# Kernel tuning notes

Hardware: AMD Instinct MI355X
Metric: run time of the kernel (lower is better)

Reference implementation:

```python
import jax, jax.numpy as jnp
import numpy as np

B, S, HID, NH, HD = 2, 8192, 768, 12, 64
BLOCK, NRAND = 64, 3


def _make_attn_indices():
    # Mirrors SparseSelfAttention.bigbird_attention index construction:
    # globals = first block + last block tokens; randoms = NRAND per block.
    rng = np.random.default_rng(0)
    glob = np.concatenate([np.arange(BLOCK), np.arange(S - BLOCK, S)])
    rand = [rng.permutation(BLOCK)[:NRAND] + i * BLOCK for i in range(S // BLOCK)]
    idx = np.unique(np.concatenate([glob] + rand))
    return jnp.asarray(idx, dtype=jnp.int32)


def setup_inputs() -> dict:
    key = jax.random.key(0)
    ks = jax.random.split(key, 6)
    w = lambda k: jax.random.normal(k, (HID, HID), jnp.float32) * 0.02
    return {
        "hidden_states": jax.random.normal(ks[0], (B, S, HID), jnp.float32),
        "attn_indices": _make_attn_indices(),
        "Wq": w(ks[1]), "bq": jnp.zeros((HID,), jnp.float32),
        "Wk": w(ks[2]), "bk": jnp.zeros((HID,), jnp.float32),
        "Wv": w(ks[3]), "bv": jnp.zeros((HID,), jnp.float32),
        "Wo": w(ks[4]), "bo": jnp.zeros((HID,), jnp.float32),
    }


def reference(hidden_states, attn_indices, Wq, bq, Wk, bk, Wv, bv, Wo, bo):
    # torch nn.Linear: y = x @ W.T + b
    heads = lambda x: x.reshape(B, S, NH, HD).transpose(0, 2, 1, 3)  # [B,H,S,d]
    q = heads(hidden_states @ Wq.T + bq)
    k = heads(hidden_states @ Wk.T + bk)
    v = heads(hidden_states @ Wv.T + bv)

    sel_q = q[:, :, attn_indices]  # gather selected queries [B,H,Nsel,d]
    scores = jnp.einsum('bhqd,bhkd->bhqk', sel_q, k) / jnp.sqrt(jnp.float32(HD))
    probs = jax.nn.softmax(scores, axis=-1)              # [B,H,Nsel,S]
    ctx = jnp.einsum('bhqk,bhkd->bhqd', probs, v)        # [B,H,Nsel,d]

    # scatter back into zeros (non-selected query positions stay zero)
    full = jnp.zeros_like(q).at[:, :, attn_indices].set(ctx)
    context = full.transpose(0, 2, 1, 3).reshape(B, S, HID)
    output = context @ Wo.T + bo
    return (output, probs)
```

## Files before the change

### kernel.cpp

```cpp
#include <hip/hip_runtime.h>
#include <hip/hip_bf16.h>

#define B_   2
#define S_   8192
#define HID_ 768
#define NH_  12
#define HD_  64

#define KC1 512
#define NC1 (S_ / KC1)
#define KC2 1024
#define NC2 (S_ / KC2)

typedef __attribute__((ext_vector_type(8))) short short8;
typedef __attribute__((ext_vector_type(4))) float f32x4;

__device__ __forceinline__ ushort f2b(float x) {
    __hip_bfloat16 h = __float2bfloat16(x);
    return *reinterpret_cast<ushort*>(&h);
}

__device__ __forceinline__ int swzb(int row, int colbyte, int rowbytes) {
    return row * rowbytes + (colbyte ^ ((row & 7) << 4));
}

__device__ __forceinline__ void glds16(const ushort* g, ushort* l) {
    __builtin_amdgcn_global_load_lds(
        (__attribute__((address_space(1))) unsigned int*)g,
        (__attribute__((address_space(3))) unsigned int*)l, 16, 0, 0);
}

__global__ void fill_bias_kernel(float* __restrict__ out, const float* __restrict__ bo) {
    const int total = B_ * S_ * (HID_ / 4);
    const float4* b4 = reinterpret_cast<const float4*>(bo);
    float4* o4 = reinterpret_cast<float4*>(out);
    for (int i = blockIdx.x * blockDim.x + threadIdx.x; i < total; i += gridDim.x * blockDim.x) {
        o4[i] = b4[i % (HID_ / 4)];
    }
}

__global__ void f32_to_bf16_kernel(const float* __restrict__ in, ushort* __restrict__ out,
                                   int n4, float scale) {
    const float4* i4 = reinterpret_cast<const float4*>(in);
    ushort4* o4 = reinterpret_cast<ushort4*>(out);
    for (int i = blockIdx.x * blockDim.x + threadIdx.x; i < n4; i += gridDim.x * blockDim.x) {
        float4 v = i4[i];
        ushort4 o;
        o.x = f2b(v.x * scale);
        o.y = f2b(v.y * scale);
        o.z = f2b(v.z * scale);
        o.w = f2b(v.w * scale);
        o4[i] = o;
    }
}

__global__ void gather_qb_kernel(const ushort* __restrict__ Hb, const int* __restrict__ idx,
                                 ushort* __restrict__ Qinb, int nq, int nqpad) {
    int m = blockIdx.x;
    int b = m / nqpad, qi = m - b * nqpad;
    uint4* dst = reinterpret_cast<uint4*>(Qinb + (size_t)m * HID_);
    if (qi < nq) {
        int srow = b * S_ + idx[qi];
        const uint4* src = reinterpret_cast<const uint4*>(Hb + (size_t)srow * HID_);
        dst[threadIdx.x] = src[threadIdx.x];
    } else {
        dst[threadIdx.x] = make_uint4(0, 0, 0, 0);
    }
}

enum { GST_KV = 0, GST_PLAIN = 1 };

template<int MODE>
__launch_bounds__(256)
__global__ void gemm_bf16_kernel(const ushort* __restrict__ A, const ushort* __restrict__ W,
                                 const float* __restrict__ bias, float bscale,
                                 ushort* __restrict__ C) {
    __shared__ __align__(16) ushort As[128 * 64];
    __shared__ __align__(16) ushort Ws[128 * 64];
    const int t = threadIdx.x;
    const int lane = t & 63, w = t >> 6;
    const int wr = w >> 1, wc = w & 1;
    const int m0 = blockIdx.x * 128;
    const int n0 = blockIdx.y * 128;

    f32x4 acc[4][4];
    #pragma unroll
    for (int i = 0; i < 4; ++i)
        #pragma unroll
        for (int j = 0; j < 4; ++j) acc[i][j] = (f32x4){0.f, 0.f, 0.f, 0.f};

    for (int k0 = 0; k0 < HID_; k0 += 64) {
        __syncthreads();
        #pragma unroll
        for (int it = 0; it < 4; ++it) {
            int sid = t + it * 256;
            int row = sid >> 3, seg = sid & 7;
            int cb = (seg * 16) ^ ((row & 7) << 4);
            glds16(A + (size_t)(m0 + row) * HID_ + k0 + cb / 2, (ushort*)((char*)As + sid * 16));
            glds16(W + (size_t)(n0 + row) * HID_ + k0 + cb / 2, (ushort*)((char*)Ws + sid * 16));
        }
        __syncthreads();

        short8 af[4][2], bf_[4][2];
        #pragma unroll
        for (int mi = 0; mi < 4; ++mi)
            #pragma unroll
            for (int kh = 0; kh < 2; ++kh)
                af[mi][kh] = *reinterpret_cast<const short8*>(
                    (char*)As + swzb(wr * 64 + mi * 16 + (lane & 15), (lane >> 4) * 16 + kh * 64, 128));
        #pragma unroll
        for (int ni = 0; ni < 4; ++ni)
            #pragma unroll
            for (int kh = 0; kh < 2; ++kh)
                bf_[ni][kh] = *reinterpret_cast<const short8*>(
                    (char*)Ws + swzb(wc * 64 + ni * 16 + (lane & 15), (lane >> 4) * 16 + kh * 64, 128));

        #pragma unroll
        for (int mi = 0; mi < 4; ++mi)
            #pragma unroll
            for (int ni = 0; ni < 4; ++ni) {
                acc[mi][ni] = __builtin_amdgcn_mfma_f32_16x16x32_bf16(af[mi][0], bf_[ni][0], acc[mi][ni], 0, 0, 0);
                acc[mi][ni] = __builtin_amdgcn_mfma_f32_16x16x32_bf16(af[mi][1], bf_[ni][1], acc[mi][ni], 0, 0, 0);
            }
    }

    float bl[4];
    #pragma unroll
    for (int ni = 0; ni < 4; ++ni)
        bl[ni] = bias[n0 + wc * 64 + ni * 16 + (lane & 15)] * bscale;

    #pragma unroll
    for (int mi = 0; mi < 4; ++mi) {
        #pragma unroll
        for (int ni = 0; ni < 4; ++ni) {
            int n = n0 + wc * 64 + ni * 16 + (lane & 15);
            #pragma unroll
            for (int r = 0; r < 4; ++r) {
                int m = m0 + wr * 64 + mi * 16 + (lane >> 4) * 4 + r;
                ushort val = f2b(acc[mi][ni][r] + bl[ni]);
                if (MODE == GST_KV) {
                    int b = m >> 13, s = m & (S_ - 1);
                    int h = n >> 6, d = n & 63;
                    C[(((size_t)(b * NH_ + h)) * S_ + s) * HD_ + d] = val;
                } else {
                    C[(size_t)m * HID_ + n] = val;
                }
            }
        }
    }
}

__launch_bounds__(256)
__global__ void gemm64_scatter(const float* __restrict__ A, const float* __restrict__ W,
                               const float* __restrict__ bias, float* __restrict__ Cf,
                               int M, const int* __restrict__ idx, int nq) {
    __shared__ float As[16][68];
    __shared__ float Ws[16][68];
    const int t  = threadIdx.x;
    const int m0 = blockIdx.x * 64;
    const int n0 = blockIdx.y * 64;
    const int tm = t >> 4, tn = t & 15;

    float acc[4][4];
    #pragma unroll
    for (int i = 0; i < 4; ++i)
        #pragma unroll
        for (int j = 0; j < 4; ++j) acc[i][j] = 0.f;

    const int fr = t >> 2, fc = t & 3;
    for (int k0 = 0; k0 < HID_; k0 += 16) {
        float4 av = make_float4(0.f, 0.f, 0.f, 0.f);
        if (m0 + fr < M) av = *reinterpret_cast<const float4*>(&A[(size_t)(m0 + fr) * HID_ + k0 + fc * 4]);
        float4 wv = *reinterpret_cast<const float4*>(&W[(size_t)(n0 + fr) * HID_ + k0 + fc * 4]);
        As[fc * 4 + 0][fr] = av.x;
        As[fc * 4 + 1][fr] = av.y;
        As[fc * 4 + 2][fr] = av.z;
        As[fc * 4 + 3][fr] = av.w;
        Ws[fc * 4 + 0][fr] = wv.x;
        Ws[fc * 4 + 1][fr] = wv.y;
        Ws[fc * 4 + 2][fr] = wv.z;
        Ws[fc * 4 + 3][fr] = wv.w;
        __syncthreads();
        #pragma unroll
        for (int kk = 0; kk < 16; ++kk) {
            float4 a4 = *reinterpret_cast<const float4*>(&As[kk][tm * 4]);
            float4 w4 = *reinterpret_cast<const float4*>(&Ws[kk][tn * 4]);
            float a[4] = {a4.x, a4.y, a4.z, a4.w};
            float ww[4] = {w4.x, w4.y, w4.z, w4.w};
            #pragma unroll
            for (int i = 0; i < 4; ++i)
                #pragma unroll
                for (int j = 0; j < 4; ++j)
                    acc[i][j] = fmaf(a[i], ww[j], acc[i][j]);
        }
        __syncthreads();
    }

    float bl[4];
    #pragma unroll
    for (int j = 0; j < 4; ++j) bl[j] = bias[n0 + tn * 4 + j];

    #pragma unroll
    for (int i = 0; i < 4; ++i) {
        int m = m0 + tm * 4 + i;
        if (m >= M) continue;
        int b = m / nq, qi = m - b * nq;
        int srow = b * S_ + idx[qi];
        float* p = &Cf[(size_t)srow * HID_ + n0 + tn * 4];
        *reinterpret_cast<float4*>(p) =
            make_float4(acc[i][0] + bl[0], acc[i][1] + bl[1], acc[i][2] + bl[2], acc[i][3] + bl[3]);
    }
}

__global__ void transpose_v_kernel(const ushort* __restrict__ V, ushort* __restrict__ Vt) {
    __shared__ ushort tile[64][72];
    int bh = blockIdx.y;
    int k0 = blockIdx.x * 64;
    int t = threadIdx.x;
    const ushort* src = V + (size_t)bh * S_ * HD_ + (size_t)k0 * HD_;
    #pragma unroll
    for (int it = 0; it < 2; ++it) {
        int sid = t + it * 256;
        int key = sid >> 3, seg = sid & 7;
        *reinterpret_cast<uint4*>(&tile[key][seg * 8]) =
            *reinterpret_cast<const uint4*>(src + (size_t)key * HD_ + seg * 8);
    }
    __syncthreads();
    ushort* dst = Vt + (size_t)bh * HD_ * S_ + k0;
    #pragma unroll
    for (int it = 0; it < 2; ++it) {
        int sid = t + it * 256;
        int d = sid >> 3, seg = sid & 7;
        ushort tmp[8];
        #pragma unroll
        for (int j = 0; j < 8; ++j) tmp[j] = tile[seg * 8 + j][d];
        *reinterpret_cast<uint4*>(dst + (size_t)d * S_ + seg * 8) = *reinterpret_cast<uint4*>(tmp);
    }
}

__launch_bounds__(512)
__global__ void attn_pass1_mfma(const ushort* __restrict__ Qsel, const ushort* __restrict__ Kb,
                                float2* __restrict__ mlp, int nq, int nqpad) {
    __shared__ __align__(16) ushort Ks[128 * 64];
    const int t = threadIdx.x;
    const int lane = t & 63, w = t >> 6;
    const int bh = blockIdx.z;
    const int b = bh / NH_, h = bh - b * NH_;
    const int q0 = blockIdx.x * 128;
    const int chunk = blockIdx.y;

    const ushort* qp = Qsel + (size_t)(b * nqpad + q0 + 16 * w + (lane & 15)) * HID_
                       + h * HD_ + (lane >> 4) * 8;
    short8 qa0 = *reinterpret_cast<const short8*>(qp);
    short8 qa1 = *reinterpret_cast<const short8*>(qp + 32);

    float m_r[4], l_r[4];
    #pragma unroll
    for (int r = 0; r < 4; ++r) { m_r[r] = -1e30f; l_r[r] = 0.f; }

    const ushort* kbase = Kb + (size_t)bh * S_ * HD_;

    for (int kb = 0; kb < KC1; kb += 128) {
        int k0 = chunk * KC1 + kb;
        __syncthreads();
        #pragma unroll
        for (int it = 0; it < 2; ++it) {
            int sid = t + it * 512;
            int row = sid >> 3, seg = sid & 7;
            int cb = (seg * 16) ^ ((row & 7) << 4);
            glds16(kbase + (size_t)(k0 + row) * HD_ + cb / 2, (ushort*)((char*)Ks + sid * 16));
        }
        __syncthreads();

        f32x4 sf[8];
        #pragma unroll
        for (int ns = 0; ns < 8; ++ns) {
            short8 b0 = *reinterpret_cast<const short8*>((char*)Ks + swzb(ns * 16 + (lane & 15), (lane >> 4) * 16, 128));
            short8 b1 = *reinterpret_cast<const short8*>((char*)Ks + swzb(ns * 16 + (lane & 15), (lane >> 4) * 16 + 64, 128));
            f32x4 acc = {0.f, 0.f, 0.f, 0.f};
            acc = __builtin_amdgcn_mfma_f32_16x16x32_bf16(qa0, b0, acc, 0, 0, 0);
            acc = __builtin_amdgcn_mfma_f32_16x16x32_bf16(qa1, b1, acc, 0, 0, 0);
            sf[ns] = acc;
        }

        #pragma unroll
        for (int r = 0; r < 4; ++r) {
            float bm = sf[0][r];
            #pragma unroll
            for (int ns = 1; ns < 8; ++ns) bm = fmaxf(bm, sf[ns][r]);
            float mn = fmaxf(m_r[r], bm);
            float sum = 0.f;
            #pragma unroll
            for (int ns = 0; ns < 8; ++ns) sum += __expf(sf[ns][r] - mn);
            l_r[r] = l_r[r] * __expf(m_r[r] - mn) + sum;
            m_r[r] = mn;
        }
    }

    #pragma unroll
    for (int r = 0; r < 4; ++r) {
        float m = m_r[r], l = l_r[r];
        #pragma unroll
        for (int off = 1; off < 16; off <<= 1) {
            float om = __shfl_xor(m, off);
            float ol = __shfl_xor(l, off);
            float mn = fmaxf(m, om);
            l = l * __expf(m - mn) + ol * __expf(om - mn);
            m = mn;
        }
        if ((lane & 15) == 0) {
            int row = q0 + 16 * w + 4 * (lane >> 4) + r;
            mlp[(size_t)chunk * (B_ * NH_ * nqpad) + (size_t)bh * nqpad + row] = make_float2(m, l);
        }
    }
}

__global__ void ml_reduce_kernel(const float2* __restrict__ mlp, float2* __restrict__ ml, int nqpad) {
    int i = blockIdx.x * blockDim.x + threadIdx.x;
    int total = B_ * NH_ * nqpad;
    if (i >= total) return;
    float m = -1e30f, l = 0.f;
    #pragma unroll
    for (int c = 0; c < NC1; ++c) {
        float2 v = mlp[(size_t)c * total + i];
        float mn = fmaxf(m, v.x);
        l = l * __expf(m - mn) + v.y * __expf(v.x - mn);
        m = mn;
    }
    ml[i] = make_float2(m, l);
}

__launch_bounds__(512)
__global__ void attn_pass2_mfma(const ushort* __restrict__ Qsel, const ushort* __restrict__ Kb,
                                const ushort* __restrict__ Vtb, const float2* __restrict__ ml,
                                float* __restrict__ probs, float* __restrict__ ctxp, int nq, int nqpad) {
    __shared__ __align__(16) ushort Ks[128 * 64];
    __shared__ __align__(16) ushort Vs[64 * 128];
    __shared__ __align__(16) ushort Ps[128 * 128];
    __shared__ float mls[128], ils[128];
    const int t = threadIdx.x;
    const int lane = t & 63, w = t >> 6;
    const int bh = blockIdx.z;
    const int b = bh / NH_, h = bh - b * NH_;
    const int q0 = blockIdx.x * 128;
    const int chunk = blockIdx.y;

    const ushort* qp = Qsel + (size_t)(b * nqpad + q0 + 16 * w + (lane & 15)) * HID_
                       + h * HD_ + (lane >> 4) * 8;
    short8 qa0 = *reinterpret_cast<const short8*>(qp);
    short8 qa1 = *reinterpret_cast<const short8*>(qp + 32);

    if (t < 128) {
        float2 v = ml[(size_t)bh * nqpad + q0 + t];
        mls[t] = v.x;
        ils[t] = 1.f / v.y;
    }

    const ushort* kbase  = Kb  + (size_t)bh * S_ * HD_;
    const ushort* vtbase = Vtb + (size_t)bh * HD_ * S_;
    const size_t prow0 = (size_t)bh * nq;

    f32x4 accc[4];
    #pragma unroll
    for (int d = 0; d < 4; ++d) accc[d] = (f32x4){0.f, 0.f, 0.f, 0.f};

    float mr[4], ilr[4];
    bool mload = false;

    for (int kb = 0; kb < KC2; kb += 128) {
        int k0 = chunk * KC2 + kb;
        __syncthreads();
        #pragma unroll
        for (int it = 0; it < 2; ++it) {
            int sid = t + it * 512;
            int row = sid >> 3, seg = sid & 7;
            int cb = (seg * 16) ^ ((row & 7) << 4);
            glds16(kbase + (size_t)(k0 + row) * HD_ + cb / 2, (ushort*)((char*)Ks + sid * 16));
        }
        #pragma unroll
        for (int it = 0; it < 2; ++it) {
            int sid = t + it * 512;
            int row = sid >> 4, seg = sid & 15;
            int cb = (seg * 16) ^ ((row & 7) << 4);
            glds16(vtbase + (size_t)row * S_ + k0 + cb / 2, (ushort*)((char*)Vs + sid * 16));
        }
        __syncthreads();
        if (!mload) {
            #pragma unroll
            for (int r = 0; r < 4; ++r) {
                int rl = 16 * w + 4 * (lane >> 4) + r;
                mr[r] = mls[rl];
                ilr[r] = ils[rl];
            }
            mload = true;
        }

        #pragma unroll
        for (int ns = 0; ns < 8; ++ns) {
            short8 b0 = *reinterpret_cast<const short8*>((char*)Ks + swzb(ns * 16 + (lane & 15), (lane >> 4) * 16, 128));
            short8 b1 = *reinterpret_cast<const short8*>((char*)Ks + swzb(ns * 16 + (lane & 15), (lane >> 4) * 16 + 64, 128));
            f32x4 acc = {0.f, 0.f, 0.f, 0.f};
            acc = __builtin_amdgcn_mfma_f32_16x16x32_bf16(qa0, b0, acc, 0, 0, 0);
            acc = __builtin_amdgcn_mfma_f32_16x16x32_bf16(qa1, b1, acc, 0, 0, 0);
            #pragma unroll
            for (int r = 0; r < 4; ++r) {
                int rl = 16 * w + 4 * (lane >> 4) + r;
                float p = __expf(acc[r] - mr[r]) * ilr[r];
                int qrow = q0 + rl;
                if (qrow < nq)
                    probs[(prow0 + qrow) * (size_t)S_ + k0 + ns * 16 + (lane & 15)] = p;
                *reinterpret_cast<ushort*>((char*)Ps + swzb(rl, (ns * 16 + (lane & 15)) * 2, 256)) = f2b(p);
            }
        }

        short8 pa[4];
        #pragma unroll
        for (int ks = 0; ks < 4; ++ks)
            pa[ks] = *reinterpret_cast<const short8*>((char*)Ps + swzb(16 * w + (lane & 15), ks * 64 + (lane >> 4) * 16, 256));
        #pragma unroll
        for (int ds = 0; ds < 4; ++ds) {
            #pragma unroll
            for (int ks = 0; ks < 4; ++ks) {
                short8 vb = *reinterpret_cast<const short8*>((char*)Vs + swzb(ds * 16 + (lane & 15), ks * 64 + (lane >> 4) * 16, 256));
                accc[ds] = __builtin_amdgcn_mfma_f32_16x16x32_bf16(pa[ks], vb, accc[ds], 0, 0, 0);
            }
        }
    }

    float* dst = ctxp + (size_t)chunk * ((size_t)B_ * nq * HID_);
    #pragma unroll
    for (int ds = 0; ds < 4; ++ds) {
        #pragma unroll
        for (int r = 0; r < 4; ++r) {
            int qrow = q0 + 16 * w + 4 * (lane >> 4) + r;
            if (qrow < nq)
                dst[(size_t)(b * nq + qrow) * HID_ + h * HD_ + ds * 16 + (lane & 15)] = accc[ds][r];
        }
    }
}

__global__ void ctx_reduce_kernel(const float* __restrict__ ctxp, float* __restrict__ ctx, int Mq) {
    const int n4 = Mq * (HID_ / 4);
    const float4* src = reinterpret_cast<const float4*>(ctxp);
    float4* dst = reinterpret_cast<float4*>(ctx);
    for (int i = blockIdx.x * blockDim.x + threadIdx.x; i < n4; i += gridDim.x * blockDim.x) {
        float4 s = make_float4(0.f, 0.f, 0.f, 0.f);
        #pragma unroll
        for (int c = 0; c < NC2; ++c) {
            float4 v = src[(size_t)c * n4 + i];
            s.x += v.x; s.y += v.y; s.z += v.z; s.w += v.w;
        }
        dst[i] = s;
    }
}

extern "C" void kernel_launch(void* const* d_in, const int* in_sizes, int n_in,
                              void* d_out, int out_size, void* d_ws, size_t ws_size,
                              hipStream_t stream) {
    const float* hidden = (const float*)d_in[0];
    const int*   idx    = (const int*)d_in[1];
    const float* Wq = (const float*)d_in[2];
    const float* bq = (const float*)d_in[3];
    const float* Wk = (const float*)d_in[4];
    const float* bk = (const float*)d_in[5];
    const float* Wv = (const float*)d_in[6];
    const float* bv = (const float*)d_in[7];
    const float* Wo = (const float*)d_in[8];
    const float* bo = (const float*)d_in[9];
    const int nq = in_sizes[1];
    const int qt128 = (nq + 127) / 128;
    const int nqpad = qt128 * 128;
    const int Mq = B_ * nq;
    const int Mqp = B_ * nqpad;

    float* out   = (float*)d_out;
    float* probs = out + (size_t)B_ * S_ * HID_;

    char* ws = (char*)d_ws;
    const size_t kvN = (size_t)B_ * NH_ * S_ * HD_;
    ushort* Hb    = (ushort*)ws;                 ws += kvN * 2;
    ushort* K_buf = (ushort*)ws;                 ws += kvN * 2;
    ushort* V_buf = (ushort*)ws;                 ws += kvN * 2;
    ushort* Vt    = (ushort*)ws;                 ws += kvN * 2;
    ushort* Wkb   = (ushort*)ws;                 ws += (size_t)HID_ * HID_ * 2;
    ushort* Wvb   = (ushort*)ws;                 ws += (size_t)HID_ * HID_ * 2;
    ushort* Wqb   = (ushort*)ws;                 ws += (size_t)HID_ * HID_ * 2;
    ushort* Qinb  = (ushort*)ws;                 ws += (size_t)Mqp * HID_ * 2;
    ushort* Qsel  = (ushort*)ws;                 ws += (size_t)Mqp * HID_ * 2;
    float*  ctxb  = (float*)ws;                  ws += (size_t)Mq * HID_ * 4;
    float*  ctxp  = (float*)ws;                  ws += (size_t)NC2 * Mq * HID_ * 4;
    float2* mlp   = (float2*)ws;                 ws += (size_t)NC1 * B_ * NH_ * nqpad * 8;
    float2* ml    = (float2*)ws;                 ws += (size_t)B_ * NH_ * nqpad * 8;

    fill_bias_kernel<<<2048, 256, 0, stream>>>(out, bo);

    f32_to_bf16_kernel<<<2048, 256, 0, stream>>>(hidden, Hb, (int)(kvN / 4), 1.0f);
    const int wn4 = HID_ * HID_ / 4;
    f32_to_bf16_kernel<<<576, 256, 0, stream>>>(Wk, Wkb, wn4, 1.0f);
    f32_to_bf16_kernel<<<576, 256, 0, stream>>>(Wv, Wvb, wn4, 1.0f);
    f32_to_bf16_kernel<<<576, 256, 0, stream>>>(Wq, Wqb, wn4, 0.125f);

    gather_qb_kernel<<<Mqp, 96, 0, stream>>>(Hb, idx, Qinb, nq, nqpad);

    dim3 gKV(B_ * S_ / 128, HID_ / 128);
    gemm_bf16_kernel<GST_KV><<<gKV, 256, 0, stream>>>(Hb, Wkb, bk, 1.0f, K_buf);
    gemm_bf16_kernel<GST_KV><<<gKV, 256, 0, stream>>>(Hb, Wvb, bv, 1.0f, V_buf);

    transpose_v_kernel<<<dim3(S_ / 64, B_ * NH_), 256, 0, stream>>>(V_buf, Vt);

    dim3 gQ(Mqp / 128, HID_ / 128);
    gemm_bf16_kernel<GST_PLAIN><<<gQ, 256, 0, stream>>>(Qinb, Wqb, bq, 0.125f, Qsel);

    dim3 gA1(nqpad / 128, NC1, B_ * NH_);
    attn_pass1_mfma<<<gA1, 512, 0, stream>>>(Qsel, K_buf, mlp, nq, nqpad);

    int totalml = B_ * NH_ * nqpad;
    ml_reduce_kernel<<<(totalml + 255) / 256, 256, 0, stream>>>(mlp, ml, nqpad);

    dim3 gA2(nqpad / 128, NC2, B_ * NH_);
    attn_pass2_mfma<<<gA2, 512, 0, stream>>>(Qsel, K_buf, Vt, ml, probs, ctxp, nq, nqpad);

    ctx_reduce_kernel<<<1024, 256, 0, stream>>>(ctxp, ctxb, Mq);

    dim3 gO((Mq + 63) / 64, HID_ / 64);
    gemm64_scatter<<<gO, 256, 0, stream>>>(ctxb, Wo, bo, out, Mq, idx, nq);
}
```

Before: 338.4 us.

## Loop all query tiles per block in attention, bf16 MFMA output GEMM, fuse weight casts

Each attention block (pass 1 and pass 2) now loops over up to four 128-row query tiles. This reuses each K/V tile loaded into shared memory across all queries instead of reloading it once per query tile. Pass 2 chunk size drops to 512 to keep enough blocks in flight. The fp32 SIMT output projection is replaced by the bf16 MFMA GEMM with a scatter epilogue, so the context reduce now emits bf16 and Wo is also converted. The four weight conversions are merged into one launch. The risks are higher register pressure and a hard cap of 512 selected queries, since more would silently drop tiles.

```diff
diff --git a/kernel.cpp b/kernel.cpp
--- a/kernel.cpp
+++ b/kernel.cpp
@@ -9,7 +9,7 @@
 
 #define KC1 512
 #define NC1 (S_ / KC1)
-#define KC2 1024
+#define KC2 512
 #define NC2 (S_ / KC2)
 
 typedef __attribute__((ext_vector_type(8))) short short8;
@@ -54,6 +54,28 @@
     }
 }
 
+__global__ void conv_weights_kernel(const float* __restrict__ Wk, const float* __restrict__ Wv,
+                                    const float* __restrict__ Wq, const float* __restrict__ Wo,
+                                    ushort* __restrict__ Wkb, ushort* __restrict__ Wvb,
+                                    ushort* __restrict__ Wqb, ushort* __restrict__ Wob) {
+    int which = blockIdx.y;
+    const float* src = which == 0 ? Wk : (which == 1 ? Wv : (which == 2 ? Wq : Wo));
+    ushort* dst = which == 0 ? Wkb : (which == 1 ? Wvb : (which == 2 ? Wqb : Wob));
+    float scale = (which == 2) ? 0.125f : 1.0f;
+    const int n4 = HID_ * HID_ / 4;
+    const float4* i4 = reinterpret_cast<const float4*>(src);
+    ushort4* o4 = reinterpret_cast<ushort4*>(dst);
+    for (int i = blockIdx.x * blockDim.x + threadIdx.x; i < n4; i += gridDim.x * blockDim.x) {
+        float4 v = i4[i];
+        ushort4 o;
+        o.x = f2b(v.x * scale);
+        o.y = f2b(v.y * scale);
+        o.z = f2b(v.z * scale);
+        o.w = f2b(v.w * scale);
+        o4[i] = o;
+    }
+}
+
 __global__ void gather_qb_kernel(const ushort* __restrict__ Hb, const int* __restrict__ idx,
                                  ushort* __restrict__ Qinb, int nq, int nqpad) {
     int m = blockIdx.x;
@@ -68,13 +90,14 @@
     }
 }
 
-enum { GST_KV = 0, GST_PLAIN = 1 };
+enum { GST_KV = 0, GST_PLAIN = 1, GST_SCATF32 = 2 };
 
 template<int MODE>
 __launch_bounds__(256)
 __global__ void gemm_bf16_kernel(const ushort* __restrict__ A, const ushort* __restrict__ W,
                                  const float* __restrict__ bias, float bscale,
-                                 ushort* __restrict__ C) {
+                                 ushort* __restrict__ C, float* __restrict__ Cf,
+                                 const int* __restrict__ idx, int nq, int Mq) {
     __shared__ __align__(16) ushort As[128 * 64];
     __shared__ __align__(16) ushort Ws[128 * 64];
     const int t = threadIdx.x;
@@ -137,78 +160,22 @@
             #pragma unroll
             for (int r = 0; r < 4; ++r) {
                 int m = m0 + wr * 64 + mi * 16 + (lane >> 4) * 4 + r;
-                ushort val = f2b(acc[mi][ni][r] + bl[ni]);
+                float fv = acc[mi][ni][r] + bl[ni];
                 if (MODE == GST_KV) {
                     int b = m >> 13, s = m & (S_ - 1);
                     int h = n >> 6, d = n & 63;
-                    C[(((size_t)(b * NH_ + h)) * S_ + s) * HD_ + d] = val;
+                    C[(((size_t)(b * NH_ + h)) * S_ + s) * HD_ + d] = f2b(fv);
+                } else if (MODE == GST_PLAIN) {
+                    C[(size_t)m * HID_ + n] = f2b(fv);
                 } else {
-                    C[(size_t)m * HID_ + n] = val;
+                    if (m < Mq) {
+                        int b = m / nq, qi = m - b * nq;
+                        int srow = b * S_ + idx[qi];
+                        Cf[(size_t)srow * HID_ + n] = fv;
+                    }
                 }
             }
         }
-    }
-}
-
-__launch_bounds__(256)
-__global__ void gemm64_scatter(const float* __restrict__ A, const float* __restrict__ W,
-                               const float* __restrict__ bias, float* __restrict__ Cf,
-                               int M, const int* __restrict__ idx, int nq) {
-    __shared__ float As[16][68];
-    __shared__ float Ws[16][68];
-    const int t  = threadIdx.x;
-    const int m0 = blockIdx.x * 64;
-    const int n0 = blockIdx.y * 64;
-    const int tm = t >> 4, tn = t & 15;
-
-    float acc[4][4];
-    #pragma unroll
-    for (int i = 0; i < 4; ++i)
-        #pragma unroll
-        for (int j = 0; j < 4; ++j) acc[i][j] = 0.f;
-
-    const int fr = t >> 2, fc = t & 3;
-    for (int k0 = 0; k0 < HID_; k0 += 16) {
-        float4 av = make_float4(0.f, 0.f, 0.f, 0.f);
-        if (m0 + fr < M) av = *reinterpret_cast<const float4*>(&A[(size_t)(m0 + fr) * HID_ + k0 + fc * 4]);
-        float4 wv = *reinterpret_cast<const float4*>(&W[(size_t)(n0 + fr) * HID_ + k0 + fc * 4]);
-        As[fc * 4 + 0][fr] = av.x;
-        As[fc * 4 + 1][fr] = av.y;
-        As[fc * 4 + 2][fr] = av.z;
-        As[fc * 4 + 3][fr] = av.w;
-        Ws[fc * 4 + 0][fr] = wv.x;
-        Ws[fc * 4 + 1][fr] = wv.y;
-        Ws[fc * 4 + 2][fr] = wv.z;
-        Ws[fc * 4 + 3][fr] = wv.w;
-        __syncthreads();
-        #pragma unroll
-        for (int kk = 0; kk < 16; ++kk) {
-            float4 a4 = *reinterpret_cast<const float4*>(&As[kk][tm * 4]);
-            float4 w4 = *reinterpret_cast<const float4*>(&Ws[kk][tn * 4]);
-            float a[4] = {a4.x, a4.y, a4.z, a4.w};
-            float ww[4] = {w4.x, w4.y, w4.z, w4.w};
-            #pragma unroll
-            for (int i = 0; i < 4; ++i)
-                #pragma unroll
-                for (int j = 0; j < 4; ++j)
-                    acc[i][j] = fmaf(a[i], ww[j], acc[i][j]);
-        }
-        __syncthreads();
-    }
-
-    float bl[4];
-    #pragma unroll
-    for (int j = 0; j < 4; ++j) bl[j] = bias[n0 + tn * 4 + j];
-
-    #pragma unroll
-    for (int i = 0; i < 4; ++i) {
-        int m = m0 + tm * 4 + i;
-        if (m >= M) continue;
-        int b = m / nq, qi = m - b * nq;
-        int srow = b * S_ + idx[qi];
-        float* p = &Cf[(size_t)srow * HID_ + n0 + tn * 4];
-        *reinterpret_cast<float4*>(p) =
-            make_float4(acc[i][0] + bl[0], acc[i][1] + bl[1], acc[i][2] + bl[2], acc[i][3] + bl[3]);
     }
 }
 
@@ -244,19 +211,26 @@
     __shared__ __align__(16) ushort Ks[128 * 64];
     const int t = threadIdx.x;
     const int lane = t & 63, w = t >> 6;
-    const int bh = blockIdx.z;
+    const int chunk = blockIdx.x, bh = blockIdx.y;
     const int b = bh / NH_, h = bh - b * NH_;
-    const int q0 = blockIdx.x * 128;
-    const int chunk = blockIdx.y;
-
-    const ushort* qp = Qsel + (size_t)(b * nqpad + q0 + 16 * w + (lane & 15)) * HID_
-                       + h * HD_ + (lane >> 4) * 8;
-    short8 qa0 = *reinterpret_cast<const short8*>(qp);
-    short8 qa1 = *reinterpret_cast<const short8*>(qp + 32);
-
-    float m_r[4], l_r[4];
-    #pragma unroll
-    for (int r = 0; r < 4; ++r) { m_r[r] = -1e30f; l_r[r] = 0.f; }
+    const int nqt = nqpad >> 7;
+
+    short8 qa[4][2];
+    #pragma unroll
+    for (int qt = 0; qt < 4; ++qt) {
+        if (qt < nqt) {
+            const ushort* qp = Qsel + (size_t)(b * nqpad + qt * 128 + 16 * w + (lane & 15)) * HID_
+                               + h * HD_ + (lane >> 4) * 8;
+            qa[qt][0] = *reinterpret_cast<const short8*>(qp);
+            qa[qt][1] = *reinterpret_cast<const short8*>(qp + 32);
+        }
+    }
+
+    float m_r[4][4], l_r[4][4];
+    #pragma unroll
+    for (int qt = 0; qt < 4; ++qt)
+        #pragma unroll
+        for (int r = 0; r < 4; ++r) { m_r[qt][r] = -1e30f; l_r[qt][r] = 0.f; }
 
     const ushort* kbase = Kb + (size_t)bh * S_ * HD_;
 
@@ -272,45 +246,59 @@
         }
         __syncthreads();
 
-        f32x4 sf[8];
+        short8 kf[8][2];
         #pragma unroll
         for (int ns = 0; ns < 8; ++ns) {
-            short8 b0 = *reinterpret_cast<const short8*>((char*)Ks + swzb(ns * 16 + (lane & 15), (lane >> 4) * 16, 128));
-            short8 b1 = *reinterpret_cast<const short8*>((char*)Ks + swzb(ns * 16 + (lane & 15), (lane >> 4) * 16 + 64, 128));
-            f32x4 acc = {0.f, 0.f, 0.f, 0.f};
-            acc = __builtin_amdgcn_mfma_f32_16x16x32_bf16(qa0, b0, acc, 0, 0, 0);
-            acc = __builtin_amdgcn_mfma_f32_16x16x32_bf16(qa1, b1, acc, 0, 0, 0);
-            sf[ns] = acc;
-        }
-
+            kf[ns][0] = *reinterpret_cast<const short8*>((char*)Ks + swzb(ns * 16 + (lane & 15), (lane >> 4) * 16, 128));
+            kf[ns][1] = *reinterpret_cast<const short8*>((char*)Ks + swzb(ns * 16 + (lane & 15), (lane >> 4) * 16 + 64, 128));
+        }
+
+        #pragma unroll
+        for (int qt = 0; qt < 4; ++qt) {
+            if (qt >= nqt) continue;
+            f32x4 sf[8];
+            __builtin_amdgcn_s_setprio(1);
+            #pragma unroll
+            for (int ns = 0; ns < 8; ++ns) {
+                f32x4 acc = {0.f, 0.f, 0.f, 0.f};
+                acc = __builtin_amdgcn_mfma_f32_16x16x32_bf16(qa[qt][0], kf[ns][0], acc, 0, 0, 0);
+                acc = __builtin_amdgcn_mfma_f32_16x16x32_bf16(qa[qt][1], kf[ns][1], acc, 0, 0, 0);
+                sf[ns] = acc;
+            }
+            __builtin_amdgcn_s_setprio(0);
+            #pragma unroll
+            for (int r = 0; r < 4; ++r) {
+                float bm = sf[0][r];
+                #pragma unroll
+                for (int ns = 1; ns < 8; ++ns) bm = fmaxf(bm, sf[ns][r]);
+                float mn = fmaxf(m_r[qt][r], bm);
+                float sum = 0.f;
+                #pragma unroll
+                for (int ns = 0; ns < 8; ++ns) sum += __expf(sf[ns][r] - mn);
+                l_r[qt][r] = l_r[qt][r] * __expf(m_r[qt][r] - mn) + sum;
+                m_r[qt][r] = mn;
+            }
+        }
+    }
+
+    #pragma unroll
+    for (int qt = 0; qt < 4; ++qt) {
+        if (qt >= nqt) continue;
         #pragma unroll
         for (int r = 0; r < 4; ++r) {
-            float bm = sf[0][r];
-            #pragma unroll
-            for (int ns = 1; ns < 8; ++ns) bm = fmaxf(bm, sf[ns][r]);
-            float mn = fmaxf(m_r[r], bm);
-            float sum = 0.f;
-            #pragma unroll
-            for (int ns = 0; ns < 8; ++ns) sum += __expf(sf[ns][r] - mn);
-            l_r[r] = l_r[r] * __expf(m_r[r] - mn) + sum;
-            m_r[r] = mn;
-        }
-    }
-
-    #pragma unroll
-    for (int r = 0; r < 4; ++r) {
-        float m = m_r[r], l = l_r[r];
-        #pragma unroll
-        for (int off = 1; off < 16; off <<= 1) {
-            float om = __shfl_xor(m, off);
-            float ol = __shfl_xor(l, off);
-            float mn = fmaxf(m, om);
-            l = l * __expf(m - mn) + ol * __expf(om - mn);
-            m = mn;
-        }
-        if ((lane & 15) == 0) {
-            int row = q0 + 16 * w + 4 * (lane >> 4) + r;
-            mlp[(size_t)chunk * (B_ * NH_ * nqpad) + (size_t)bh * nqpad + row] = make_float2(m, l);
+            float m = m_r[qt][r], l = l_r[qt][r];
+            #pragma unroll
+            for (int off = 1; off < 16; off <<= 1) {
+                float om = __shfl_xor(m, off);
+                float ol = __shfl_xor(l, off);
+                float mn = fmaxf(m, om);
+                l = l * __expf(m - mn) + ol * __expf(om - mn);
+                m = mn;
+            }
+            if ((lane & 15) == 0) {
+                int row = qt * 128 + 16 * w + 4 * (lane >> 4) + r;
+                mlp[(size_t)chunk * (B_ * NH_ * nqpad) + (size_t)bh * nqpad + row] = make_float2(m, l);
+            }
         }
     }
 }
@@ -337,21 +325,26 @@
     __shared__ __align__(16) ushort Ks[128 * 64];
     __shared__ __align__(16) ushort Vs[64 * 128];
     __shared__ __align__(16) ushort Ps[128 * 128];
-    __shared__ float mls[128], ils[128];
+    __shared__ float mls[512], ils[512];
     const int t = threadIdx.x;
     const int lane = t & 63, w = t >> 6;
-    const int bh = blockIdx.z;
+    const int chunk = blockIdx.x, bh = blockIdx.y;
     const int b = bh / NH_, h = bh - b * NH_;
-    const int q0 = blockIdx.x * 128;
-    const int chunk = blockIdx.y;
-
-    const ushort* qp = Qsel + (size_t)(b * nqpad + q0 + 16 * w + (lane & 15)) * HID_
-                       + h * HD_ + (lane >> 4) * 8;
-    short8 qa0 = *reinterpret_cast<const short8*>(qp);
-    short8 qa1 = *reinterpret_cast<const short8*>(qp + 32);
-
-    if (t < 128) {
-        float2 v = ml[(size_t)bh * nqpad + q0 + t];
+    const int nqt = nqpad >> 7;
+
+    short8 qa[4][2];
+    #pragma unroll
+    for (int qt = 0; qt < 4; ++qt) {
+        if (qt < nqt) {
+            const ushort* qp = Qsel + (size_t)(b * nqpad + qt * 128 + 16 * w + (lane & 15)) * HID_
+                               + h * HD_ + (lane >> 4) * 8;
+            qa[qt][0] = *reinterpret_cast<const short8*>(qp);
+            qa[qt][1] = *reinterpret_cast<const short8*>(qp + 32);
+        }
+    }
+
+    if (t < nqpad) {
+        float2 v = ml[(size_t)bh * nqpad + t];
         mls[t] = v.x;
         ils[t] = 1.f / v.y;
     }
@@ -360,12 +353,11 @@
     const ushort* vtbase = Vtb + (size_t)bh * HD_ * S_;
     const size_t prow0 = (size_t)bh * nq;
 
-    f32x4 accc[4];
-    #pragma unroll
-    for (int d = 0; d < 4; ++d) accc[d] = (f32x4){0.f, 0.f, 0.f, 0.f};
-
-    float mr[4], ilr[4];
-    bool mload = false;
+    f32x4 accc[4][4];
+    #pragma unroll
+    for (int qt = 0; qt < 4; ++qt)
+        #pragma unroll
+        for (int d = 0; d < 4; ++d) accc[qt][d] = (f32x4){0.f, 0.f, 0.f, 0.f};
 
     for (int kb = 0; kb < KC2; kb += 128) {
         int k0 = chunk * KC2 + kb;
@@ -385,64 +377,71 @@
             glds16(vtbase + (size_t)row * S_ + k0 + cb / 2, (ushort*)((char*)Vs + sid * 16));
         }
         __syncthreads();
-        if (!mload) {
+
+        #pragma unroll
+        for (int qt = 0; qt < 4; ++qt) {
+            if (qt >= nqt) continue;
+            float mrq[4], ilq[4];
             #pragma unroll
             for (int r = 0; r < 4; ++r) {
-                int rl = 16 * w + 4 * (lane >> 4) + r;
-                mr[r] = mls[rl];
-                ilr[r] = ils[rl];
-            }
-            mload = true;
-        }
-
-        #pragma unroll
-        for (int ns = 0; ns < 8; ++ns) {
-            short8 b0 = *reinterpret_cast<const short8*>((char*)Ks + swzb(ns * 16 + (lane & 15), (lane >> 4) * 16, 128));
-            short8 b1 = *reinterpret_cast<const short8*>((char*)Ks + swzb(ns * 16 + (lane & 15), (lane >> 4) * 16 + 64, 128));
-            f32x4 acc = {0.f, 0.f, 0.f, 0.f};
-            acc = __builtin_amdgcn_mfma_f32_16x16x32_bf16(qa0, b0, acc, 0, 0, 0);
-            acc = __builtin_amdgcn_mfma_f32_16x16x32_bf16(qa1, b1, acc, 0, 0, 0);
+                int row = qt * 128 + 16 * w + 4 * (lane >> 4) + r;
+                mrq[r] = mls[row];
+                ilq[r] = ils[row];
+            }
+            __builtin_amdgcn_s_setprio(1);
+            #pragma unroll
+            for (int ns = 0; ns < 8; ++ns) {
+                short8 b0 = *reinterpret_cast<const short8*>((char*)Ks + swzb(ns * 16 + (lane & 15), (lane >> 4) * 16, 128));
+                short8 b1 = *reinterpret_cast<const short8*>((char*)Ks + swzb(ns * 16 + (lane & 15), (lane >> 4) * 16 + 64, 128));
+                f32x4 acc = {0.f, 0.f, 0.f, 0.f};
+                acc = __builtin_amdgcn_mfma_f32_16x16x32_bf16(qa[qt][0], b0, acc, 0, 0, 0);
+                acc = __builtin_amdgcn_mfma_f32_16x16x32_bf16(qa[qt][1], b1, acc, 0, 0, 0);
+                #pragma unroll
+                for (int r = 0; r < 4; ++r) {
+                    int rl = 16 * w + 4 * (lane >> 4) + r;
+                    float p = __expf(acc[r] - mrq[r]) * ilq[r];
+                    int qrow = qt * 128 + rl;
+                    if (qrow < nq)
+                        probs[(prow0 + qrow) * (size_t)S_ + k0 + ns * 16 + (lane & 15)] = p;
+                    *reinterpret_cast<ushort*>((char*)Ps + swzb(rl, (ns * 16 + (lane & 15)) * 2, 256)) = f2b(p);
+                }
+            }
+            short8 pa[4];
+            #pragma unroll
+            for (int ks = 0; ks < 4; ++ks)
+                pa[ks] = *reinterpret_cast<const short8*>((char*)Ps + swzb(16 * w + (lane & 15), ks * 64 + (lane >> 4) * 16, 256));
+            #pragma unroll
+            for (int ds = 0; ds < 4; ++ds) {
+                #pragma unroll
+                for (int ks = 0; ks < 4; ++ks) {
+                    short8 vb = *reinterpret_cast<const short8*>((char*)Vs + swzb(ds * 16 + (lane & 15), ks * 64 + (lane >> 4) * 16, 256));
+                    accc[qt][ds] = __builtin_amdgcn_mfma_f32_16x16x32_bf16(pa[ks], vb, accc[qt][ds], 0, 0, 0);
+                }
+            }
+            __builtin_amdgcn_s_setprio(0);
+        }
+    }
+
+    float* dst = ctxp + (size_t)chunk * ((size_t)B_ * nq * HID_);
+    #pragma unroll
+    for (int qt = 0; qt < 4; ++qt) {
+        if (qt >= nqt) continue;
+        #pragma unroll
+        for (int ds = 0; ds < 4; ++ds) {
             #pragma unroll
             for (int r = 0; r < 4; ++r) {
-                int rl = 16 * w + 4 * (lane >> 4) + r;
-                float p = __expf(acc[r] - mr[r]) * ilr[r];
-                int qrow = q0 + rl;
+                int qrow = qt * 128 + 16 * w + 4 * (lane >> 4) + r;
                 if (qrow < nq)
-                    probs[(prow0 + qrow) * (size_t)S_ + k0 + ns * 16 + (lane & 15)] = p;
-                *reinterpret_cast<ushort*>((char*)Ps + swzb(rl, (ns * 16 + (lane & 15)) * 2, 256)) = f2b(p);
-            }
-        }
-
-        short8 pa[4];
-        #pragma unroll
-        for (int ks = 0; ks < 4; ++ks)
-            pa[ks] = *reinterpret_cast<const short8*>((char*)Ps + swzb(16 * w + (lane & 15), ks * 64 + (lane >> 4) * 16, 256));
-        #pragma unroll
-        for (int ds = 0; ds < 4; ++ds) {
-            #pragma unroll
-            for (int ks = 0; ks < 4; ++ks) {
-                short8 vb = *reinterpret_cast<const short8*>((char*)Vs + swzb(ds * 16 + (lane & 15), ks * 64 + (lane >> 4) * 16, 256));
-                accc[ds] = __builtin_amdgcn_mfma_f32_16x16x32_bf16(pa[ks], vb, accc[ds], 0, 0, 0);
-            }
-        }
-    }
-
-    float* dst = ctxp + (size_t)chunk * ((size_t)B_ * nq * HID_);
-    #pragma unroll
-    for (int ds = 0; ds < 4; ++ds) {
-        #pragma unroll
-        for (int r = 0; r < 4; ++r) {
-            int qrow = q0 + 16 * w + 4 * (lane >> 4) + r;
-            if (qrow < nq)
-                dst[(size_t)(b * nq + qrow) * HID_ + h * HD_ + ds * 16 + (lane & 15)] = accc[ds][r];
-        }
-    }
-}
-
-__global__ void ctx_reduce_kernel(const float* __restrict__ ctxp, float* __restrict__ ctx, int Mq) {
+                    dst[(size_t)(b * nq + qrow) * HID_ + h * HD_ + ds * 16 + (lane & 15)] = accc[qt][ds][r];
+            }
+        }
+    }
+}
+
+__global__ void ctx_reduce_kernel(const float* __restrict__ ctxp, ushort* __restrict__ ctxb, int Mq) {
     const int n4 = Mq * (HID_ / 4);
     const float4* src = reinterpret_cast<const float4*>(ctxp);
-    float4* dst = reinterpret_cast<float4*>(ctx);
+    ushort4* dst = reinterpret_cast<ushort4*>(ctxb);
     for (int i = blockIdx.x * blockDim.x + threadIdx.x; i < n4; i += gridDim.x * blockDim.x) {
         float4 s = make_float4(0.f, 0.f, 0.f, 0.f);
         #pragma unroll
@@ -450,7 +449,9 @@
             float4 v = src[(size_t)c * n4 + i];
             s.x += v.x; s.y += v.y; s.z += v.z; s.w += v.w;
         }
-        dst[i] = s;
+        ushort4 o;
+        o.x = f2b(s.x); o.y = f2b(s.y); o.z = f2b(s.z); o.w = f2b(s.w);
+        dst[i] = o;
     }
 }
 
@@ -485,9 +486,10 @@
     ushort* Wkb   = (ushort*)ws;                 ws += (size_t)HID_ * HID_ * 2;
     ushort* Wvb   = (ushort*)ws;                 ws += (size_t)HID_ * HID_ * 2;
     ushort* Wqb   = (ushort*)ws;                 ws += (size_t)HID_ * HID_ * 2;
+    ushort* Wob   = (ushort*)ws;                 ws += (size_t)HID_ * HID_ * 2;
     ushort* Qinb  = (ushort*)ws;                 ws += (size_t)Mqp * HID_ * 2;
     ushort* Qsel  = (ushort*)ws;                 ws += (size_t)Mqp * HID_ * 2;
-    float*  ctxb  = (float*)ws;                  ws += (size_t)Mq * HID_ * 4;
+    ushort* ctxb  = (ushort*)ws;                 ws += (size_t)Mqp * HID_ * 2;
     float*  ctxp  = (float*)ws;                  ws += (size_t)NC2 * Mq * HID_ * 4;
     float2* mlp   = (float2*)ws;                 ws += (size_t)NC1 * B_ * NH_ * nqpad * 8;
     float2* ml    = (float2*)ws;                 ws += (size_t)B_ * NH_ * nqpad * 8;
@@ -495,33 +497,30 @@
     fill_bias_kernel<<<2048, 256, 0, stream>>>(out, bo);
 
     f32_to_bf16_kernel<<<2048, 256, 0, stream>>>(hidden, Hb, (int)(kvN / 4), 1.0f);
-    const int wn4 = HID_ * HID_ / 4;
-    f32_to_bf16_kernel<<<576, 256, 0, stream>>>(Wk, Wkb, wn4, 1.0f);
-    f32_to_bf16_kernel<<<576, 256, 0, stream>>>(Wv, Wvb, wn4, 1.0f);
-    f32_to_bf16_kernel<<<576, 256, 0, stream>>>(Wq, Wqb, wn4, 0.125f);
+    conv_weights_kernel<<<dim3(192, 4), 256, 0, stream>>>(Wk, Wv, Wq, Wo, Wkb, Wvb, Wqb, Wob);
 
     gather_qb_kernel<<<Mqp, 96, 0, stream>>>(Hb, idx, Qinb, nq, nqpad);
 
     dim3 gKV(B_ * S_ / 128, HID_ / 128);
-    gemm_bf16_kernel<GST_KV><<<gKV, 256, 0, stream>>>(Hb, Wkb, bk, 1.0f, K_buf);
-    gemm_bf16_kernel<GST_KV><<<gKV, 256, 0, stream>>>(Hb, Wvb, bv, 1.0f, V_buf);
+    gemm_bf16_kernel<GST_KV><<<gKV, 256, 0, stream>>>(Hb, Wkb, bk, 1.0f, K_buf, nullptr, nullptr, 0, 0);
+    gemm_bf16_kernel<GST_KV><<<gKV, 256, 0, stream>>>(Hb, Wvb, bv, 1.0f, V_buf, nullptr, nullptr, 0, 0);
 
     transpose_v_kernel<<<dim3(S_ / 64, B_ * NH_), 256, 0, stream>>>(V_buf, Vt);
 
     dim3 gQ(Mqp / 128, HID_ / 128);
-    gemm_bf16_kernel<GST_PLAIN><<<gQ, 256, 0, stream>>>(Qinb, Wqb, bq, 0.125f, Qsel);
-
-    dim3 gA1(nqpad / 128, NC1, B_ * NH_);
+    gemm_bf16_kernel<GST_PLAIN><<<gQ, 256, 0, stream>>>(Qinb, Wqb, bq, 0.125f, Qsel, nullptr, nullptr, 0, 0);
+
+    dim3 gA1(NC1, B_ * NH_);
     attn_pass1_mfma<<<gA1, 512, 0, stream>>>(Qsel, K_buf, mlp, nq, nqpad);
 
     int totalml = B_ * NH_ * nqpad;
     ml_reduce_kernel<<<(totalml + 255) / 256, 256, 0, stream>>>(mlp, ml, nqpad);
 
-    dim3 gA2(nqpad / 128, NC2, B_ * NH_);
+    dim3 gA2(NC2, B_ * NH_);
     attn_pass2_mfma<<<gA2, 512, 0, stream>>>(Qsel, K_buf, Vt, ml, probs, ctxp, nq, nqpad);
 
     ctx_reduce_kernel<<<1024, 256, 0, stream>>>(ctxp, ctxb, Mq);
 
-    dim3 gO((Mq + 63) / 64, HID_ / 64);
-    gemm64_scatter<<<gO, 256, 0, stream>>>(ctxb, Wo, bo, out, Mq, idx, nq);
-}
+    dim3 gO(Mqp / 128, HID_ / 128);
+    gemm_bf16_kernel<GST_SCATF32><<<gO, 256, 0, stream>>>(ctxb, Wob, bo, 1.0f, nullptr, out, idx, nq, Mq);
+}
```

Result: faster. 329.4 us (-2.6%).
